# Kernel tuning notes

Measured on AMD Instinct MI355X. Metric: run time of the kernel, lower is better.

Reference implementation:

```python
import jax, jax.numpy as jnp
import numpy as np

B, S, HE, HD = 32, 2048, 1024, 1024

def setup_inputs() -> dict:
    key = jax.random.key(0)
    k1, k2, k3, k4, k5 = jax.random.split(key, 5)
    enc_hiddens = jax.random.normal(k1, (B, S, HE), dtype=jnp.float32)
    dec_hidden = jax.random.normal(k2, (B, HD), dtype=jnp.float32)
    mask = jax.random.randint(k3, (B, S), 0, 2).astype(bool)  # True = masked out
    # params init uniform(-0.05, 0.05) as in init_weights
    W = jax.random.uniform(k4, (HD, HE + HD), dtype=jnp.float32, minval=-0.05, maxval=0.05)
    V = jax.random.uniform(k5, (1, HD), dtype=jnp.float32, minval=-0.05, maxval=0.05)
    return {"enc_hiddens": enc_hiddens, "dec_hidden": dec_hidden, "mask": mask, "W": W, "V": V}

def reference(enc_hiddens, dec_hidden, mask, W, V):
    # e = V^T tanh(W [enc; dec]) -- split W to avoid materializing the concat:
    # W @ [enc;dec] == W_enc @ enc + W_dec @ dec (same math, fused-friendly)
    HE_ = enc_hiddens.shape[-1]
    W_enc, W_dec = W[:, :HE_], W[:, HE_:]
    h = jnp.tanh(jnp.einsum('bse,de->bsd', enc_hiddens, W_enc)
                 + jnp.einsum('be,de->bd', dec_hidden, W_dec)[:, None, :])  # [B,S,HD]
    scores = jnp.einsum('bsd,od->bs', h, V)  # [B,S] (o==1 squeezed)
    scores = jnp.where(mask, -jnp.inf, scores)
    attn = jax.nn.softmax(scores, axis=1)[:, None, :]  # [B,1,S]
    ctx = jnp.einsum('bos,bse->be', attn, enc_hiddens)  # squeeze of bmm -> [B,HE]
    return (ctx, attn)
```

## Files before the change

### kernel.cpp

```cpp
#include <hip/hip_runtime.h>
#include <hip/hip_bf16.h>
#include <math.h>

#define BB 32
#define SS 2048
#define HE 1024
#define HD 1024
#define WROW (HE + HD)

typedef __attribute__((ext_vector_type(8))) short bf16x8;
typedef __attribute__((ext_vector_type(4))) float f32x4;
typedef __attribute__((ext_vector_type(8))) unsigned short u16x8;

__device__ __forceinline__ unsigned short f2bf(float f) {
    union { float f; unsigned u; } v; v.f = f;
    unsigned r = v.u + 0x7fffu + ((v.u >> 16) & 1u);
    return (unsigned short)(r >> 16);
}

__device__ __forceinline__ unsigned int pk2(float x, float y) {
    union { __hip_bfloat162 h; unsigned int u; } c;
    c.h = __float22bfloat162_rn(float2{x, y});
    return c.u;
}

#define LGKM0()  asm volatile("s_waitcnt lgkmcnt(0)" ::: "memory")
#define BAR()    asm volatile("s_barrier" ::: "memory")

__global__ __launch_bounds__(256) void k_cvt_wfrag(const float* __restrict__ W,
                                                   unsigned short* __restrict__ wf) {
    int i = blockIdx.x * 256 + threadIdx.x;
    int d = i >> 7;
    int c = i & 127;
    const float4* src = (const float4*)(W + (size_t)d * WROW + c * 8);
    float4 a = src[0], b2 = src[1];
    u16x8 o;
    o[0] = f2bf(a.x);  o[1] = f2bf(a.y);  o[2] = f2bf(a.z);  o[3] = f2bf(a.w);
    o[4] = f2bf(b2.x); o[5] = f2bf(b2.y); o[6] = f2bf(b2.z); o[7] = f2bf(b2.w);
    int ksg = c >> 2, hi = c & 3;
    int l   = (d & 15) + 16 * hi;
    int g   = d >> 4;
    *(u16x8*)(wf + ((size_t)(g * 32 + ksg) * 64 + l) * 8) = o;
}

__global__ __launch_bounds__(256) void k_projdec2(const float* __restrict__ dec,
                                                  const float* __restrict__ W,
                                                  float* __restrict__ proj) {
    const int tid = threadIdx.x;
    const int dl = tid >> 6;
    const int b  = (tid >> 1) & 31;
    const int hf = tid & 1;
    const int d  = blockIdx.x * 4 + dl;
    const float* wrow = W + (size_t)d * WROW + HE + hf * 512;
    const float* dv   = dec + b * HD + hf * 512;
    float s = 0.f;
    #pragma unroll 4
    for (int e = 0; e < 512; e += 4) {
        float4 w4 = *(const float4*)(wrow + e);
        float4 x4 = *(const float4*)(dv + e);
        s += w4.x * x4.x + w4.y * x4.y + w4.z * x4.z + w4.w * x4.w;
    }
    s += __shfl_xor(s, 1, 64);
    if (hf == 0) proj[b * HD + d] = s;
}

__global__ __launch_bounds__(512, 1) void k_scores_mfma8b(
        const float* __restrict__ enc,
        const unsigned short* __restrict__ wf,
        const float* __restrict__ V,
        const float* __restrict__ proj,
        float* __restrict__ psc) {
    __shared__ unsigned short SM[32768];

    const int tid = threadIdx.x;
    const int wv = tid >> 6, ln = tid & 63, l15 = ln & 15, lg = ln >> 4;
    const int wr = wv >> 2, wc = wv & 3;

    const int lid  = (blockIdx.x & 7) * 128 + (blockIdx.x >> 3);
    const int trow = lid >> 2, nb = lid & 3;
    const int t0   = trow * 256;
    const int b    = t0 >> 11;

    f32x4 acc[8][4];
    #pragma unroll
    for (int m = 0; m < 8; m++)
        #pragma unroll
        for (int n = 0; n < 4; n++) acc[m][n] = (f32x4){0.f, 0.f, 0.f, 0.f};

    float4 areg[4][2];
    bf16x8 bg0[4], bg1[4];

    #define LOAD_A(k) do { \
        _Pragma("unroll") \
        for (int p = 0; p < 4; p++) { \
            const float4* g_ = (const float4*)(enc + (size_t)(t0 + p * 64 + (tid >> 3)) * 1024 + (k) + (tid & 7) * 8); \
            areg[p][0] = g_[0]; areg[p][1] = g_[1]; \
        } } while (0)

    #define CVTW_A(buf) do { \
        _Pragma("unroll") \
        for (int p = 0; p < 4; p++) { \
            int row_ = p * 64 + (tid >> 3); \
            union { u16x8 s; uint4 u; } pk_; \
            pk_.u.x = pk2(areg[p][0].x, areg[p][0].y); \
            pk_.u.y = pk2(areg[p][0].z, areg[p][0].w); \
            pk_.u.z = pk2(areg[p][1].x, areg[p][1].y); \
            pk_.u.w = pk2(areg[p][1].z, areg[p][1].w); \
            *(u16x8*)&SM[(buf) * 16384 + row_ * 64 + (((tid & 7) ^ (row_ & 7)) << 3)] = pk_.s; \
        } } while (0)

    #define LOADB(bgx, tt, ksl) do { \
        _Pragma("unroll") \
        for (int n = 0; n < 4; n++) { \
            int g_ = nb * 16 + wc * 4 + n; \
            bgx[n] = *(const bf16x8*)(wf + ((size_t)(g_ * 32 + (tt) * 2 + (ksl)) * 64 + ln) * 8); \
        } } while (0)

    #define RD_A(af, Ac, mb, ks) do { \
        _Pragma("unroll") \
        for (int m = 0; m < 4; m++) { \
            int row_ = wr * 128 + (mb) + m * 16 + l15; \
            af[m] = *(const bf16x8*)&(Ac)[row_ * 64 + ((((ks) + lg) ^ (row_ & 7)) << 3)]; \
        } } while (0)

    #define MFMA44(mo, bg, af) do { \
        __builtin_amdgcn_s_setprio(1); \
        _Pragma("unroll") \
        for (int m = 0; m < 4; m++) \
            _Pragma("unroll") \
            for (int n = 0; n < 4; n++) \
                acc[(mo) + m][n] = __builtin_amdgcn_mfma_f32_16x16x32_bf16(af[m], bg[n], acc[(mo) + m][n], 0, 0, 0); \
        __builtin_amdgcn_s_setprio(0); } while (0)

    LOADB(bg0, 0, 0); LOADB(bg1, 0, 1);
    LOAD_A(0);
    CVTW_A(0);
    LOAD_A(64);
    LGKM0(); BAR();

    for (int t = 0; t < 16; ++t) {
        const int cur = t & 1, nxt = cur ^ 1;
        const unsigned short* Ac = SM + cur * 16384;
        bf16x8 af[4];

        RD_A(af, Ac, 0, 0);
        MFMA44(0, bg0, af);
        RD_A(af, Ac, 64, 0);
        MFMA44(4, bg0, af);

        if (t < 15) {
            LOADB(bg0, t + 1, 0);
            CVTW_A(nxt);
            if (t < 14) LOAD_A((t + 2) * 64);
        }

        RD_A(af, Ac, 0, 4);
        MFMA44(0, bg1, af);
        RD_A(af, Ac, 64, 4);
        MFMA44(4, bg1, af);

        if (t < 15) {
            LOADB(bg1, t + 1, 1);
            LGKM0(); BAR();
        }
    }
    #undef LOAD_A
    #undef CVTW_A
    #undef LOADB
    #undef RD_A
    #undef MFMA44

    float sc[8][4];
    #pragma unroll
    for (int m = 0; m < 8; m++)
        #pragma unroll
        for (int j = 0; j < 4; j++) sc[m][j] = 0.f;
    #pragma unroll
    for (int n = 0; n < 4; n++) {
        int d = nb * 256 + wc * 64 + n * 16 + l15;
        float pd  = proj[b * 1024 + d];
        float vv  = V[d];
        float vv2 = 2.f * vv;
        #pragma unroll
        for (int m = 0; m < 8; m++)
            #pragma unroll
            for (int j = 0; j < 4; j++) {
                float y  = acc[m][n][j] + pd;
                float e2 = __expf(2.f * y);
                float r  = __builtin_amdgcn_rcpf(e2 + 1.f);
                sc[m][j] += vv - vv2 * r;
            }
    }

    __syncthreads();
    float* red = (float*)SM;
    #pragma unroll
    for (int m = 0; m < 8; m++)
        #pragma unroll
        for (int j = 0; j < 4; j++) {
            int tok = wr * 128 + m * 16 + lg * 4 + j;
            int col = wc * 16 + l15;
            red[tok * 64 + ((col + tok) & 63)] = sc[m][j];
        }
    __syncthreads();
    if (tid < 256) {
        float s = 0.f;
        #pragma unroll
        for (int x = 0; x < 64; x++) s += red[tid * 64 + ((x + tid) & 63)];
        psc[nb * 65536 + t0 + tid] = s;
    }
}

__global__ __launch_bounds__(256) void k_softmax_p(const float* __restrict__ psc,
                                                   const int* __restrict__ mask,
                                                   float* __restrict__ attn) {
    __shared__ float sred[256];
    const int b = blockIdx.x, tid = threadIdx.x;
    float vals[8];
    int   msk[8];
    float lmax = -1e30f;
    #pragma unroll
    for (int i = 0; i < 8; i++) {
        int s = tid + i * 256;
        float v = 0.f;
        #pragma unroll
        for (int z = 0; z < 4; z++) v += psc[z * 65536 + b * SS + s];
        vals[i] = v;
        msk[i]  = mask[b * SS + s];
        if (!msk[i]) lmax = fmaxf(lmax, vals[i]);
    }
    sred[tid] = lmax; __syncthreads();
    for (int off = 128; off > 0; off >>= 1) {
        if (tid < off) sred[tid] = fmaxf(sred[tid], sred[tid + off]);
        __syncthreads();
    }
    float m = sred[0];
    __syncthreads();
    float ex[8];
    float lsum = 0.f;
    #pragma unroll
    for (int i = 0; i < 8; i++) {
        ex[i] = msk[i] ? 0.f : __expf(vals[i] - m);
        lsum += ex[i];
    }
    sred[tid] = lsum; __syncthreads();
    for (int off = 128; off > 0; off >>= 1) {
        if (tid < off) sred[tid] += sred[tid + off];
        __syncthreads();
    }
    float inv = 1.f / sred[0];
    #pragma unroll
    for (int i = 0; i < 8; i++) attn[b * SS + tid + i * 256] = ex[i] * inv;
}

__global__ __launch_bounds__(256) void k_ctx_part(const float* __restrict__ enc,
                                                  const float* __restrict__ attn,
                                                  float* __restrict__ pctx) {
    const int b = blockIdx.x, z = blockIdx.y, tid = threadIdx.x;
    float4 acc = {0.f, 0.f, 0.f, 0.f};
    const float4* e4 = (const float4*)(enc + ((size_t)b * SS + z * 64) * HE);
    const float*  ar = attn + b * SS + z * 64;
    for (int s = 0; s < 64; s++) {
        float a = ar[s];
        if (a != 0.f) {
            float4 v = e4[(size_t)s * 256 + tid];
            acc.x += a * v.x; acc.y += a * v.y; acc.z += a * v.z; acc.w += a * v.w;
        }
    }
    *(float4*)(pctx + ((size_t)z * 32 + b) * 1024 + tid * 4) = acc;
}

__global__ __launch_bounds__(256) void k_ctx_red(const float* __restrict__ pctx,
                                                 float* __restrict__ ctx) {
    int i = blockIdx.x * 256 + threadIdx.x;
    float s = 0.f;
    #pragma unroll
    for (int z = 0; z < 32; z++) s += pctx[z * 32768 + i];
    ctx[i] = s;
}

__global__ __launch_bounds__(256) void k_scores_f32(const float* __restrict__ enc,
                                                    const float* __restrict__ W,
                                                    const float* __restrict__ V,
                                                    const float* __restrict__ proj,
                                                    float* __restrict__ scores) {
    __shared__ float As[64][20];
    __shared__ float Bs[64][20];
    __shared__ float red[64][17];
    const int t0 = blockIdx.x * 64;
    const int b  = t0 >> 11;
    const int tid = threadIdx.x;
    const int tx = tid & 15, ty = tid >> 4;
    const int lrow = tid >> 2, lc4 = (tid & 3) * 4;
    float sc[4] = {0.f, 0.f, 0.f, 0.f};
    for (int n0 = 0; n0 < HD; n0 += 64) {
        float C[4][4] = {};
        for (int k0 = 0; k0 < HE; k0 += 16) {
            *(float4*)&As[lrow][lc4] = *(const float4*)(enc + (size_t)(t0 + lrow) * HE + k0 + lc4);
            *(float4*)&Bs[lrow][lc4] = *(const float4*)(W + (size_t)(n0 + lrow) * WROW + k0 + lc4);
            __syncthreads();
            #pragma unroll
            for (int k4 = 0; k4 < 16; k4 += 4) {
                float4 a[4], bb[4];
                #pragma unroll
                for (int i = 0; i < 4; i++) a[i]  = *(float4*)&As[ty * 4 + i][k4];
                #pragma unroll
                for (int j = 0; j < 4; j++) bb[j] = *(float4*)&Bs[tx * 4 + j][k4];
                #pragma unroll
                for (int i = 0; i < 4; i++)
                    #pragma unroll
                    for (int j = 0; j < 4; j++)
                        C[i][j] += a[i].x * bb[j].x + a[i].y * bb[j].y +
                                   a[i].z * bb[j].z + a[i].w * bb[j].w;
            }
            __syncthreads();
        }
        #pragma unroll
        for (int j = 0; j < 4; j++) {
            int d = n0 + tx * 4 + j;
            float pd = proj[b * HD + d];
            float v  = V[d];
            #pragma unroll
            for (int i = 0; i < 4; i++) {
                float y  = C[i][j] + pd;
                float e2 = __expf(2.f * y);
                sc[i] += v * (1.f - 2.f / (e2 + 1.f));
            }
        }
    }
    #pragma unroll
    for (int i = 0; i < 4; i++) red[ty * 4 + i][tx] = sc[i];
    __syncthreads();
    if (tid < 64) {
        float s = 0.f;
        #pragma unroll
        for (int x = 0; x < 16; x++) s += red[tid][x];
        scores[t0 + tid] = s;
    }
}

__global__ __launch_bounds__(256) void k_softmax_f32(float* __restrict__ sc_attn,
                                                     const int* __restrict__ mask) {
    __shared__ float sred[256];
    const int b = blockIdx.x, tid = threadIdx.x;
    float vals[8]; int msk[8];
    float lmax = -1e30f;
    #pragma unroll
    for (int i = 0; i < 8; i++) {
        int s = tid + i * 256;
        vals[i] = sc_attn[b * SS + s];
        msk[i]  = mask[b * SS + s];
        if (!msk[i]) lmax = fmaxf(lmax, vals[i]);
    }
    sred[tid] = lmax; __syncthreads();
    for (int off = 128; off > 0; off >>= 1) {
        if (tid < off) sred[tid] = fmaxf(sred[tid], sred[tid + off]);
        __syncthreads();
    }
    float m = sred[0];
    __syncthreads();
    float ex[8]; float lsum = 0.f;
    #pragma unroll
    for (int i = 0; i < 8; i++) { ex[i] = msk[i] ? 0.f : __expf(vals[i] - m); lsum += ex[i]; }
    sred[tid] = lsum; __syncthreads();
    for (int off = 128; off > 0; off >>= 1) {
        if (tid < off) sred[tid] += sred[tid + off];
        __syncthreads();
    }
    float inv = 1.f / sred[0];
    #pragma unroll
    for (int i = 0; i < 8; i++) sc_attn[b * SS + tid + i * 256] = ex[i] * inv;
}

__global__ __launch_bounds__(256) void k_ctx_atomic(const float* __restrict__ enc,
                                                    const float* __restrict__ attn,
                                                    float* __restrict__ ctx) {
    const int b = blockIdx.x;
    const int e = blockIdx.y * 256 + threadIdx.x;
    const int s0 = blockIdx.z * 256;
    float sum = 0.f;
    for (int s = s0; s < s0 + 256; s++)
        sum += attn[b * SS + s] * enc[((size_t)b * SS + s) * HE + e];
    atomicAdd(&ctx[b * HE + e], sum);
}

extern "C" void kernel_launch(void* const* d_in, const int* in_sizes, int n_in,
                              void* d_out, int out_size, void* d_ws, size_t ws_size,
                              hipStream_t stream) {
    const float* enc  = (const float*)d_in[0];
    const float* dec  = (const float*)d_in[1];
    const int*   mask = (const int*)d_in[2];
    const float* W    = (const float*)d_in[3];
    const float* V    = (const float*)d_in[4];

    float* out  = (float*)d_out;
    float* ctx  = out;
    float* attn = out + BB * HE;

    const size_t WF_OFF = 0, PROJ_OFF = 2097152, PSC_OFF = PROJ_OFF + 131072,
                 PCTX_OFF = PSC_OFF + 1048576, WS_NEED = PCTX_OFF + 4194304;
    if (ws_size >= WS_NEED) {
        char* w = (char*)d_ws;
        unsigned short* wf = (unsigned short*)(w + WF_OFF);
        float* proj        = (float*)(w + PROJ_OFF);
        float* psc         = (float*)(w + PSC_OFF);
        float* pctx        = (float*)(w + PCTX_OFF);

        k_cvt_wfrag<<<512, 256, 0, stream>>>(W, wf);
        k_projdec2<<<256, 256, 0, stream>>>(dec, W, proj);
        k_scores_mfma8b<<<1024, 512, 0, stream>>>(enc, wf, V, proj, psc);
        k_softmax_p<<<BB, 256, 0, stream>>>(psc, mask, attn);
        k_ctx_part<<<dim3(BB, 32), 256, 0, stream>>>(enc, attn, pctx);
        k_ctx_red<<<128, 256, 0, stream>>>(pctx, ctx);
    } else {
        float* proj  = ctx;
        float* score = attn;
        k_projdec2<<<256, 256, 0, stream>>>(dec, W, proj);
        k_scores_f32<<<(BB * SS) / 64, 256, 0, stream>>>(enc, W, V, proj, score);
        k_softmax_f32<<<BB, 256, 0, stream>>>(score, mask);
        hipMemsetAsync(ctx, 0, (size_t)BB * HE * sizeof(float), stream);
        k_ctx_atomic<<<dim3(BB, HE / 256, 8), 256, 0, stream>>>(enc, attn, ctx);
    }
}
```

Baseline: 214.2 us.

## Retile score GEMM to 64 tokens by full hidden width per block

Each block of the score kernel now computes 64 tokens across all 1024 hidden columns, where it previously computed 256 tokens by 256 columns. The four-way column split, and the reduction of four partial scores in the softmax kernel, both go away. Each encoder row is now read and converted once rather than by four blocks, and the smaller LDS footprint lets two blocks share a CU. The cost is twice as many per-wave global loads of the weight fragments and more accumulator registers per wave, which may raise register pressure and L2 traffic for the weights.

```diff
diff --git a/kernel.cpp b/kernel.cpp
--- a/kernel.cpp
+++ b/kernel.cpp
@@ -64,75 +64,70 @@
     if (hf == 0) proj[b * HD + d] = s;
 }
 
-__global__ __launch_bounds__(512, 1) void k_scores_mfma8b(
+__global__ __launch_bounds__(512, 2) void k_scores_mfma8b(
         const float* __restrict__ enc,
         const unsigned short* __restrict__ wf,
         const float* __restrict__ V,
         const float* __restrict__ proj,
         float* __restrict__ psc) {
-    __shared__ unsigned short SM[32768];
+    __shared__ unsigned short SM[16384];
 
     const int tid = threadIdx.x;
     const int wv = tid >> 6, ln = tid & 63, l15 = ln & 15, lg = ln >> 4;
-    const int wr = wv >> 2, wc = wv & 3;
 
     const int lid  = (blockIdx.x & 7) * 128 + (blockIdx.x >> 3);
-    const int trow = lid >> 2, nb = lid & 3;
-    const int t0   = trow * 256;
+    const int t0   = lid * 64;
     const int b    = t0 >> 11;
 
-    f32x4 acc[8][4];
-    #pragma unroll
-    for (int m = 0; m < 8; m++)
-        #pragma unroll
-        for (int n = 0; n < 4; n++) acc[m][n] = (f32x4){0.f, 0.f, 0.f, 0.f};
-
-    float4 areg[4][2];
-    bf16x8 bg0[4], bg1[4];
+    f32x4 acc[4][8];
+    #pragma unroll
+    for (int m = 0; m < 4; m++)
+        #pragma unroll
+        for (int n = 0; n < 8; n++) acc[m][n] = (f32x4){0.f, 0.f, 0.f, 0.f};
+
+    float4 areg[2];
+    bf16x8 bgA[4], bgB[4], bgC[4], bgD[4];
 
     #define LOAD_A(k) do { \
-        _Pragma("unroll") \
-        for (int p = 0; p < 4; p++) { \
-            const float4* g_ = (const float4*)(enc + (size_t)(t0 + p * 64 + (tid >> 3)) * 1024 + (k) + (tid & 7) * 8); \
-            areg[p][0] = g_[0]; areg[p][1] = g_[1]; \
-        } } while (0)
+        const float4* g_ = (const float4*)(enc + (size_t)(t0 + (tid >> 3)) * 1024 + (k) + (tid & 7) * 8); \
+        areg[0] = g_[0]; areg[1] = g_[1]; \
+    } while (0)
 
     #define CVTW_A(buf) do { \
-        _Pragma("unroll") \
-        for (int p = 0; p < 4; p++) { \
-            int row_ = p * 64 + (tid >> 3); \
-            union { u16x8 s; uint4 u; } pk_; \
-            pk_.u.x = pk2(areg[p][0].x, areg[p][0].y); \
-            pk_.u.y = pk2(areg[p][0].z, areg[p][0].w); \
-            pk_.u.z = pk2(areg[p][1].x, areg[p][1].y); \
-            pk_.u.w = pk2(areg[p][1].z, areg[p][1].w); \
-            *(u16x8*)&SM[(buf) * 16384 + row_ * 64 + (((tid & 7) ^ (row_ & 7)) << 3)] = pk_.s; \
-        } } while (0)
-
-    #define LOADB(bgx, tt, ksl) do { \
+        int row_ = tid >> 3; \
+        union { u16x8 s; uint4 u; } pk_; \
+        pk_.u.x = pk2(areg[0].x, areg[0].y); \
+        pk_.u.y = pk2(areg[0].z, areg[0].w); \
+        pk_.u.z = pk2(areg[1].x, areg[1].y); \
+        pk_.u.w = pk2(areg[1].z, areg[1].w); \
+        *(u16x8*)&SM[(buf) * 4096 + row_ * 64 + (((tid & 7) ^ (row_ & 7)) << 3)] = pk_.s; \
+    } while (0)
+
+    #define LOADB(bgx, tt, ksl, no) do { \
         _Pragma("unroll") \
         for (int n = 0; n < 4; n++) { \
-            int g_ = nb * 16 + wc * 4 + n; \
+            int g_ = wv * 8 + (no) + n; \
             bgx[n] = *(const bf16x8*)(wf + ((size_t)(g_ * 32 + (tt) * 2 + (ksl)) * 64 + ln) * 8); \
         } } while (0)
 
-    #define RD_A(af, Ac, mb, ks) do { \
+    #define RD_A(af, Ac, ks) do { \
         _Pragma("unroll") \
         for (int m = 0; m < 4; m++) { \
-            int row_ = wr * 128 + (mb) + m * 16 + l15; \
+            int row_ = m * 16 + l15; \
             af[m] = *(const bf16x8*)&(Ac)[row_ * 64 + ((((ks) + lg) ^ (row_ & 7)) << 3)]; \
         } } while (0)
 
-    #define MFMA44(mo, bg, af) do { \
+    #define MFMA4N(no, bg, af) do { \
         __builtin_amdgcn_s_setprio(1); \
         _Pragma("unroll") \
         for (int m = 0; m < 4; m++) \
             _Pragma("unroll") \
             for (int n = 0; n < 4; n++) \
-                acc[(mo) + m][n] = __builtin_amdgcn_mfma_f32_16x16x32_bf16(af[m], bg[n], acc[(mo) + m][n], 0, 0, 0); \
+                acc[m][(no) + n] = __builtin_amdgcn_mfma_f32_16x16x32_bf16(af[m], bg[n], acc[m][(no) + n], 0, 0, 0); \
         __builtin_amdgcn_s_setprio(0); } while (0)
 
-    LOADB(bg0, 0, 0); LOADB(bg1, 0, 1);
+    LOADB(bgA, 0, 0, 0); LOADB(bgB, 0, 0, 4);
+    LOADB(bgC, 0, 1, 0); LOADB(bgD, 0, 1, 4);
     LOAD_A(0);
     CVTW_A(0);
     LOAD_A(64);
@@ -140,27 +135,27 @@
 
     for (int t = 0; t < 16; ++t) {
         const int cur = t & 1, nxt = cur ^ 1;
-        const unsigned short* Ac = SM + cur * 16384;
+        const unsigned short* Ac = SM + cur * 4096;
         bf16x8 af[4];
 
-        RD_A(af, Ac, 0, 0);
-        MFMA44(0, bg0, af);
-        RD_A(af, Ac, 64, 0);
-        MFMA44(4, bg0, af);
+        RD_A(af, Ac, 0);
+        MFMA4N(0, bgA, af);
+        MFMA4N(4, bgB, af);
 
         if (t < 15) {
-            LOADB(bg0, t + 1, 0);
+            LOADB(bgA, t + 1, 0, 0);
+            LOADB(bgB, t + 1, 0, 4);
             CVTW_A(nxt);
             if (t < 14) LOAD_A((t + 2) * 64);
         }
 
-        RD_A(af, Ac, 0, 4);
-        MFMA44(0, bg1, af);
-        RD_A(af, Ac, 64, 4);
-        MFMA44(4, bg1, af);
+        RD_A(af, Ac, 4);
+        MFMA4N(0, bgC, af);
+        MFMA4N(4, bgD, af);
 
         if (t < 15) {
-            LOADB(bg1, t + 1, 1);
+            LOADB(bgC, t + 1, 1, 0);
+            LOADB(bgD, t + 1, 1, 4);
             LGKM0(); BAR();
         }
     }
@@ -168,21 +163,21 @@
     #undef CVTW_A
     #undef LOADB
     #undef RD_A
-    #undef MFMA44
-
-    float sc[8][4];
-    #pragma unroll
-    for (int m = 0; m < 8; m++)
+    #undef MFMA4N
+
+    float sc[4][4];
+    #pragma unroll
+    for (int m = 0; m < 4; m++)
         #pragma unroll
         for (int j = 0; j < 4; j++) sc[m][j] = 0.f;
     #pragma unroll
-    for (int n = 0; n < 4; n++) {
-        int d = nb * 256 + wc * 64 + n * 16 + l15;
+    for (int n = 0; n < 8; n++) {
+        int d = wv * 128 + n * 16 + l15;
         float pd  = proj[b * 1024 + d];
         float vv  = V[d];
         float vv2 = 2.f * vv;
         #pragma unroll
-        for (int m = 0; m < 8; m++)
+        for (int m = 0; m < 4; m++)
             #pragma unroll
             for (int j = 0; j < 4; j++) {
                 float y  = acc[m][n][j] + pd;
@@ -195,19 +190,19 @@
     __syncthreads();
     float* red = (float*)SM;
     #pragma unroll
-    for (int m = 0; m < 8; m++)
+    for (int m = 0; m < 4; m++)
         #pragma unroll
         for (int j = 0; j < 4; j++) {
-            int tok = wr * 128 + m * 16 + lg * 4 + j;
-            int col = wc * 16 + l15;
-            red[tok * 64 + ((col + tok) & 63)] = sc[m][j];
+            int tok = m * 16 + lg * 4 + j;
+            int col = wv * 16 + l15;
+            red[tok * 128 + ((col + tok) & 127)] = sc[m][j];
         }
     __syncthreads();
-    if (tid < 256) {
+    if (tid < 64) {
         float s = 0.f;
         #pragma unroll
-        for (int x = 0; x < 64; x++) s += red[tid * 64 + ((x + tid) & 63)];
-        psc[nb * 65536 + t0 + tid] = s;
+        for (int x = 0; x < 128; x++) s += red[tid * 128 + ((x + tid) & 127)];
+        psc[t0 + tid] = s;
     }
 }
 
@@ -222,10 +217,7 @@
     #pragma unroll
     for (int i = 0; i < 8; i++) {
         int s = tid + i * 256;
-        float v = 0.f;
-        #pragma unroll
-        for (int z = 0; z < 4; z++) v += psc[z * 65536 + b * SS + s];
-        vals[i] = v;
+        vals[i] = psc[b * SS + s];
         msk[i]  = mask[b * SS + s];
         if (!msk[i]) lmax = fmaxf(lmax, vals[i]);
     }
```

Result: faster. 204.7 us (-4.4%).
